# Performance work log

Hardware: AMD Instinct MI355X
Metric: run time of the kernel (lower is better)

## Reference

```python
import jax, jax.numpy as jnp
import numpy as np

NUM_EMBEDDINGS = 1024
EMBEDDING_DIM = 128
COMMITMENT_COST = 0.25


def setup_inputs() -> dict:
    key = jax.random.key(0)
    k1, k2 = jax.random.split(key)
    z = jax.random.normal(k1, (16, EMBEDDING_DIM, 64, 64), dtype=jnp.float32)
    # torch init: uniform(-1/num_embeddings, 1/num_embeddings)
    lim = 1.0 / NUM_EMBEDDINGS
    embedding = jax.random.uniform(
        k2, (NUM_EMBEDDINGS, EMBEDDING_DIM), dtype=jnp.float32,
        minval=-lim, maxval=lim)
    return {"z": z, "embedding": embedding}


def reference(z, embedding):
    b, c, h, w = z.shape  # c == EMBEDDING_DIM
    # (b, h, w, c) -> (b*h*w, c)
    z_flat = jnp.transpose(z, (0, 2, 3, 1)).reshape(-1, c)
    # squared euclidean distances: ||z||^2 + ||e||^2 - 2 z e^T  -> (N, K)
    distances = (jnp.sum(z_flat ** 2, axis=-1, keepdims=True)
                 + jnp.sum(embedding ** 2, axis=-1)[None, :]
                 - 2.0 * jnp.matmul(z_flat, embedding.T))
    encoding_indices = jnp.argmin(distances, axis=-1)  # (N,) int
    z_q = embedding[encoding_indices].reshape(b, h, w, c)
    z_q = jnp.transpose(z_q, (0, 3, 1, 2))  # (b, c, h, w)
    commitment_loss = COMMITMENT_COST * jnp.sum(
        (jax.lax.stop_gradient(z_q) - z) ** 2)
    codebook_loss = jnp.sum((z_q - jax.lax.stop_gradient(z)) ** 2)
    loss = codebook_loss + commitment_loss
    # straight-through estimator
    z_q_st = z + jax.lax.stop_gradient(z_q - z)
    return (z_q_st, loss, encoding_indices, commitment_loss, codebook_loss)
```

## Files before the change

kernel.cpp:

```cpp
#include <hip/hip_runtime.h>
#include <hip/hip_bf16.h>

#define C 128
#define HW 4096
#define NPOS 65536
#define K 1024
#define MB 128
#define NBLK (NPOS/MB)
#define RS 136
#define RSB 320
#define CHK 64
#define NCH (K/CHK)
#define CHB (CHK*RSB)

#define ZQ_OFF 0
#define LOSS_OFF 8388608
#define IDX_OFF 8388609
#define COMMIT_OFF 8454145
#define CODE_OFF 8454146

#define WS_IMG_OFF 8192

typedef __bf16 bf16x8 __attribute__((ext_vector_type(8)));
typedef float f32x4 __attribute__((ext_vector_type(4)));

__global__ void vq_prep(const float* __restrict__ emb, unsigned char* __restrict__ img,
                        float* __restrict__ S) {
    int k = blockIdx.x;
    int l = threadIdx.x;
    if (k == 0 && l == 0) { S[0] = 0.0f; ((unsigned int*)S)[1] = 0u; }
    float v0 = emb[k * C + l];
    float v1 = emb[k * C + 64 + l];
    __hip_bfloat16 h0 = __float2bfloat16(v0);
    __hip_bfloat16 h1 = __float2bfloat16(v1);
    unsigned short* row = (unsigned short*)(img + (size_t)k * RSB);
    row[l] = *(unsigned short*)&h0;
    row[64 + l] = *(unsigned short*)&h1;
    float s = v0 * v0 + v1 * v1;
    #pragma unroll
    for (int off = 32; off; off >>= 1) s += __shfl_down(s, off);
    if (l == 0) *(float*)(img + (size_t)k * RSB + 256) = s + 1.0f;
}

__global__ __launch_bounds__(256, 2)
void vq_main(const float* __restrict__ z, const float* __restrict__ emb,
             const unsigned char* __restrict__ img,
             float* __restrict__ out, float* __restrict__ S) {
    __shared__ unsigned short zt[MB * RS];
    __shared__ unsigned int wbest[4][MB];
    __shared__ unsigned short idxs[MB];
    __shared__ float lred[4];

    const int t = threadIdx.x;
    const int w = t >> 6;
    const int lane = t & 63;
    const int nn = lane & 15;
    const int q = lane >> 4;

    const int blk = blockIdx.x;
    const int n0g = blk * MB;
    const int b = n0g >> 12;
    const int hw0 = n0g & (HW - 1);
    const float* zg = z + (size_t)b * C * HW + hw0;

    {
        int pos = t & (MB - 1);
        int c0b = (t >> 7) * 64;
        #pragma unroll
        for (int i = 0; i < 16; ++i) {
            int c0 = c0b + i * 4;
            float f0 = zg[(size_t)(c0 + 0) * HW + pos];
            float f1 = zg[(size_t)(c0 + 1) * HW + pos];
            float f2 = zg[(size_t)(c0 + 2) * HW + pos];
            float f3 = zg[(size_t)(c0 + 3) * HW + pos];
            __hip_bfloat16 h0 = __float2bfloat16(f0), h1 = __float2bfloat16(f1),
                           h2 = __float2bfloat16(f2), h3 = __float2bfloat16(f3);
            ushort4 pk;
            pk.x = *(unsigned short*)&h0; pk.y = *(unsigned short*)&h1;
            pk.z = *(unsigned short*)&h2; pk.w = *(unsigned short*)&h3;
            *(ushort4*)&zt[pos * RS + c0] = pk;
        }
    }
    __syncthreads();

    bf16x8 a[8][4];
    #pragma unroll
    for (int mt = 0; mt < 8; ++mt)
        #pragma unroll
        for (int ks = 0; ks < 4; ++ks)
            a[mt][ks] = *(bf16x8*)&zt[(mt * 16 + nn) * RS + ks * 32 + q * 8];

    unsigned int best[8][4];
    #pragma unroll
    for (int mt = 0; mt < 8; ++mt)
        #pragma unroll
        for (int r = 0; r < 4; ++r) best[mt][r] = 0xFFFFFFFFu;

    const int row = w * 16 + nn;
    const unsigned char* pb = img + (size_t)row * RSB + q * 16;
    const unsigned char* pe = img + (size_t)row * RSB + 256;

    bf16x8 bcur[4];
    #pragma unroll
    for (int ks = 0; ks < 4; ++ks) bcur[ks] = *(const bf16x8*)(pb + ks * 64);
    float ecur = *(const float*)pe;

    #pragma unroll 2
    for (int ch = 0; ch < NCH; ++ch) {
        const int step = (ch + 1 < NCH) ? CHB : 0;
        bf16x8 bnxt[4];
        #pragma unroll
        for (int ks = 0; ks < 4; ++ks) bnxt[ks] = *(const bf16x8*)(pb + step + ks * 64);
        float enxt = *(const float*)(pe + step);

        const unsigned int code = (unsigned int)(ch * CHK + row);

        f32x4 acc[8];
        #pragma unroll
        for (int mt = 0; mt < 8; ++mt) acc[mt] = (f32x4){0.f, 0.f, 0.f, 0.f};
        #pragma unroll
        for (int ks = 0; ks < 4; ++ks)
            #pragma unroll
            for (int mt = 0; mt < 8; ++mt)
                acc[mt] = __builtin_amdgcn_mfma_f32_16x16x32_bf16(a[mt][ks], bcur[ks], acc[mt], 0, 0, 0);

        #pragma unroll
        for (int mt = 0; mt < 8; ++mt)
            #pragma unroll
            for (int r = 0; r < 4; ++r) {
                float s = fmaf(acc[mt][r], -2.0f, ecur);
                unsigned int u = (__float_as_uint(s) & ~1023u) | code;
                best[mt][r] = min(best[mt][r], u);
            }

        #pragma unroll
        for (int ks = 0; ks < 4; ++ks) bcur[ks] = bnxt[ks];
        ecur = enxt;
        pb += CHB; pe += CHB;
    }

    #pragma unroll
    for (int mt = 0; mt < 8; ++mt)
        #pragma unroll
        for (int r = 0; r < 4; ++r) {
            unsigned int v = best[mt][r];
            v = min(v, (unsigned int)__shfl_xor((int)v, 1));
            v = min(v, (unsigned int)__shfl_xor((int)v, 2));
            v = min(v, (unsigned int)__shfl_xor((int)v, 4));
            v = min(v, (unsigned int)__shfl_xor((int)v, 8));
            if (nn == 0) wbest[w][mt * 16 + q * 4 + r] = v;
        }
    __syncthreads();

    if (t < MB) {
        unsigned int v = min(min(wbest[0][t], wbest[1][t]), min(wbest[2][t], wbest[3][t]));
        unsigned int code = v & 1023u;
        idxs[t] = (unsigned short)code;
        out[IDX_OFF + n0g + t] = (float)code;
    }
    __syncthreads();

    {
        int pos = t & (MB - 1);
        int c0b = (t >> 7) * 64;
        int myidx = idxs[pos];
        const float* erow = emb + (size_t)myidx * C;
        float* og = out + ZQ_OFF + (size_t)b * C * HW + hw0;
        float ls = 0.f;
        #pragma unroll
        for (int i = 0; i < 16; ++i) {
            int c0 = c0b + i * 4;
            float4 ev = *(const float4*)&erow[c0];
            ushort4 zz = *(ushort4*)&zt[pos * RS + c0];
            float z0 = __uint_as_float((unsigned int)zz.x << 16);
            float z1 = __uint_as_float((unsigned int)zz.y << 16);
            float z2 = __uint_as_float((unsigned int)zz.z << 16);
            float z3 = __uint_as_float((unsigned int)zz.w << 16);
            float d0 = z0 - ev.x, d1 = z1 - ev.y, d2 = z2 - ev.z, d3 = z3 - ev.w;
            ls += d0 * d0 + d1 * d1 + d2 * d2 + d3 * d3;
            og[(size_t)(c0 + 0) * HW + pos] = ev.x;
            og[(size_t)(c0 + 1) * HW + pos] = ev.y;
            og[(size_t)(c0 + 2) * HW + pos] = ev.z;
            og[(size_t)(c0 + 3) * HW + pos] = ev.w;
        }
        #pragma unroll
        for (int off = 32; off; off >>= 1) ls += __shfl_down(ls, off);
        if (lane == 0) lred[w] = ls;
    }
    __syncthreads();

    if (t == 0) {
        float bs = lred[0] + lred[1] + lred[2] + lred[3];
        atomicAdd(S, bs);
        __threadfence();
        unsigned int old = atomicAdd((unsigned int*)S + 1, 1u);
        if (old == NBLK - 1) {
            __threadfence();
            float s = atomicAdd(S, 0.0f);
            out[LOSS_OFF] = 1.25f * s;
            out[COMMIT_OFF] = 0.25f * s;
            out[CODE_OFF] = s;
        }
    }
}

extern "C" void kernel_launch(void* const* d_in, const int* in_sizes, int n_in,
                              void* d_out, int out_size, void* d_ws, size_t ws_size,
                              hipStream_t stream) {
    const float* z = (const float*)d_in[0];
    const float* emb = (const float*)d_in[1];
    float* out = (float*)d_out;
    float* S = (float*)d_ws;
    unsigned char* img = (unsigned char*)d_ws + WS_IMG_OFF;

    vq_prep<<<K, 64, 0, stream>>>(emb, img, S);
    vq_main<<<NBLK, 256, 0, stream>>>(z, emb, img, out, S);
}
```

Baseline: 135.1 us.

## Split VQ block across 8 waves in a 2x4 grid and add final loss kernel

Doubles threads per block to 512 and splits the 128 positions across two wave rows, so each wave keeps 4 M-tiles of A fragments instead of 8. This cuts register pressure and allows more waves per CU. It also removes the software prefetch of codebook B fragments and replaces the last-block atomic counter with a separate one-thread finalization kernel. The risks are exposed global load latency without prefetch, duplicated codebook loads across wave rows, and one extra kernel launch.

```diff
diff --git a/kernel.cpp b/kernel.cpp
--- a/kernel.cpp
+++ b/kernel.cpp
@@ -28,7 +28,7 @@
                         float* __restrict__ S) {
     int k = blockIdx.x;
     int l = threadIdx.x;
-    if (k == 0 && l == 0) { S[0] = 0.0f; ((unsigned int*)S)[1] = 0u; }
+    if (k == 0 && l == 0) S[0] = 0.0f;
     float v0 = emb[k * C + l];
     float v1 = emb[k * C + 64 + l];
     __hip_bfloat16 h0 = __float2bfloat16(v0);
@@ -42,20 +42,22 @@
     if (l == 0) *(float*)(img + (size_t)k * RSB + 256) = s + 1.0f;
 }
 
-__global__ __launch_bounds__(256, 2)
+__global__ __launch_bounds__(512, 4)
 void vq_main(const float* __restrict__ z, const float* __restrict__ emb,
              const unsigned char* __restrict__ img,
              float* __restrict__ out, float* __restrict__ S) {
-    __shared__ unsigned short zt[MB * RS];
+    __shared__ __align__(16) unsigned short zt[MB * RS];
     __shared__ unsigned int wbest[4][MB];
     __shared__ unsigned short idxs[MB];
-    __shared__ float lred[4];
+    __shared__ float lred[8];
 
     const int t = threadIdx.x;
     const int w = t >> 6;
     const int lane = t & 63;
     const int nn = lane & 15;
     const int q = lane >> 4;
+    const int wm = w >> 2;
+    const int wn = w & 3;
 
     const int blk = blockIdx.x;
     const int n0g = blk * MB;
@@ -65,9 +67,9 @@
 
     {
         int pos = t & (MB - 1);
-        int c0b = (t >> 7) * 64;
-        #pragma unroll
-        for (int i = 0; i < 16; ++i) {
+        int c0b = (t >> 7) * 32;
+        #pragma unroll
+        for (int i = 0; i < 8; ++i) {
             int c0 = c0b + i * 4;
             float f0 = zg[(size_t)(c0 + 0) * HW + pos];
             float f1 = zg[(size_t)(c0 + 1) * HW + pos];
@@ -83,64 +85,52 @@
     }
     __syncthreads();
 
-    bf16x8 a[8][4];
-    #pragma unroll
-    for (int mt = 0; mt < 8; ++mt)
+    bf16x8 a[4][4];
+    #pragma unroll
+    for (int mt = 0; mt < 4; ++mt)
         #pragma unroll
         for (int ks = 0; ks < 4; ++ks)
-            a[mt][ks] = *(bf16x8*)&zt[(mt * 16 + nn) * RS + ks * 32 + q * 8];
-
-    unsigned int best[8][4];
-    #pragma unroll
-    for (int mt = 0; mt < 8; ++mt)
+            a[mt][ks] = *(bf16x8*)&zt[(wm * 64 + mt * 16 + nn) * RS + ks * 32 + q * 8];
+
+    unsigned int best[4][4];
+    #pragma unroll
+    for (int mt = 0; mt < 4; ++mt)
         #pragma unroll
         for (int r = 0; r < 4; ++r) best[mt][r] = 0xFFFFFFFFu;
 
-    const int row = w * 16 + nn;
-    const unsigned char* pb = img + (size_t)row * RSB + q * 16;
-    const unsigned char* pe = img + (size_t)row * RSB + 256;
-
-    bf16x8 bcur[4];
-    #pragma unroll
-    for (int ks = 0; ks < 4; ++ks) bcur[ks] = *(const bf16x8*)(pb + ks * 64);
-    float ecur = *(const float*)pe;
-
-    #pragma unroll 2
+    const unsigned char* pb = img + (size_t)(wn * 16 + nn) * RSB + q * 16;
+    const unsigned char* pe = img + (size_t)(wn * 16 + nn) * RSB + 256;
+
     for (int ch = 0; ch < NCH; ++ch) {
-        const int step = (ch + 1 < NCH) ? CHB : 0;
-        bf16x8 bnxt[4];
-        #pragma unroll
-        for (int ks = 0; ks < 4; ++ks) bnxt[ks] = *(const bf16x8*)(pb + step + ks * 64);
-        float enxt = *(const float*)(pe + step);
-
-        const unsigned int code = (unsigned int)(ch * CHK + row);
-
-        f32x4 acc[8];
-        #pragma unroll
-        for (int mt = 0; mt < 8; ++mt) acc[mt] = (f32x4){0.f, 0.f, 0.f, 0.f};
+        bf16x8 bf[4];
+        #pragma unroll
+        for (int ks = 0; ks < 4; ++ks)
+            bf[ks] = *(const bf16x8*)(pb + ks * 64);
+        const float en1 = *(const float*)pe;
+        const unsigned int code = (unsigned int)(ch * CHK + wn * 16 + nn);
+
+        f32x4 acc[4];
+        #pragma unroll
+        for (int mt = 0; mt < 4; ++mt) acc[mt] = (f32x4){0.f, 0.f, 0.f, 0.f};
         #pragma unroll
         for (int ks = 0; ks < 4; ++ks)
             #pragma unroll
-            for (int mt = 0; mt < 8; ++mt)
-                acc[mt] = __builtin_amdgcn_mfma_f32_16x16x32_bf16(a[mt][ks], bcur[ks], acc[mt], 0, 0, 0);
-
-        #pragma unroll
-        for (int mt = 0; mt < 8; ++mt)
+            for (int mt = 0; mt < 4; ++mt)
+                acc[mt] = __builtin_amdgcn_mfma_f32_16x16x32_bf16(a[mt][ks], bf[ks], acc[mt], 0, 0, 0);
+
+        #pragma unroll
+        for (int mt = 0; mt < 4; ++mt)
             #pragma unroll
             for (int r = 0; r < 4; ++r) {
-                float s = fmaf(acc[mt][r], -2.0f, ecur);
+                float s = fmaf(acc[mt][r], -2.0f, en1);
                 unsigned int u = (__float_as_uint(s) & ~1023u) | code;
                 best[mt][r] = min(best[mt][r], u);
             }
-
-        #pragma unroll
-        for (int ks = 0; ks < 4; ++ks) bcur[ks] = bnxt[ks];
-        ecur = enxt;
         pb += CHB; pe += CHB;
     }
 
     #pragma unroll
-    for (int mt = 0; mt < 8; ++mt)
+    for (int mt = 0; mt < 4; ++mt)
         #pragma unroll
         for (int r = 0; r < 4; ++r) {
             unsigned int v = best[mt][r];
@@ -148,7 +138,7 @@
             v = min(v, (unsigned int)__shfl_xor((int)v, 2));
             v = min(v, (unsigned int)__shfl_xor((int)v, 4));
             v = min(v, (unsigned int)__shfl_xor((int)v, 8));
-            if (nn == 0) wbest[w][mt * 16 + q * 4 + r] = v;
+            if (nn == 0) wbest[wn][wm * 64 + mt * 16 + q * 4 + r] = v;
         }
     __syncthreads();
 
@@ -162,13 +152,13 @@
 
     {
         int pos = t & (MB - 1);
-        int c0b = (t >> 7) * 64;
+        int c0b = (t >> 7) * 32;
         int myidx = idxs[pos];
         const float* erow = emb + (size_t)myidx * C;
         float* og = out + ZQ_OFF + (size_t)b * C * HW + hw0;
         float ls = 0.f;
         #pragma unroll
-        for (int i = 0; i < 16; ++i) {
+        for (int i = 0; i < 8; ++i) {
             int c0 = c0b + i * 4;
             float4 ev = *(const float4*)&erow[c0];
             ushort4 zz = *(ushort4*)&zt[pos * RS + c0];
@@ -188,20 +178,19 @@
         if (lane == 0) lred[w] = ls;
     }
     __syncthreads();
-
     if (t == 0) {
-        float bs = lred[0] + lred[1] + lred[2] + lred[3];
+        float bs = 0.f;
+        #pragma unroll
+        for (int i = 0; i < 8; ++i) bs += lred[i];
         atomicAdd(S, bs);
-        __threadfence();
-        unsigned int old = atomicAdd((unsigned int*)S + 1, 1u);
-        if (old == NBLK - 1) {
-            __threadfence();
-            float s = atomicAdd(S, 0.0f);
-            out[LOSS_OFF] = 1.25f * s;
-            out[COMMIT_OFF] = 0.25f * s;
-            out[CODE_OFF] = s;
-        }
-    }
+    }
+}
+
+__global__ void vq_final(const float* __restrict__ S, float* __restrict__ out) {
+    float s = *S;
+    out[LOSS_OFF] = 1.25f * s;
+    out[COMMIT_OFF] = 0.25f * s;
+    out[CODE_OFF] = s;
 }
 
 extern "C" void kernel_launch(void* const* d_in, const int* in_sizes, int n_in,
@@ -214,5 +203,6 @@
     unsigned char* img = (unsigned char*)d_ws + WS_IMG_OFF;
 
     vq_prep<<<K, 64, 0, stream>>>(emb, img, S);
-    vq_main<<<NBLK, 256, 0, stream>>>(z, emb, img, out, S);
-}
+    vq_main<<<NBLK, 512, 0, stream>>>(z, emb, img, out, S);
+    vq_final<<<1, 1, 0, stream>>>(S, out);
+}
```

New measurement: 121.2 us. 1.12x faster.
